# Optimization experiments

Measured on AMD Instinct MI355X. Metric: run time of the kernel, lower is better.

The kernel has to match this reference:

```python
import jax, jax.numpy as jnp
import numpy as np

N, E = 50000, 800000
D_IN, D_HID, D_OUT = 128, 128, 64
BN_EPS = 1e-5
GEN_EPS = 1e-7


def _lin_init(k, fan_in, shape):
    lim = 1.0 / np.sqrt(fan_in)
    return jax.random.uniform(k, shape, minval=-lim, maxval=lim, dtype=jnp.float32)


def setup_inputs() -> dict:
    key = jax.random.key(0)
    ks = jax.random.split(key, 12)
    x = jax.random.normal(ks[0], (N, D_IN), dtype=jnp.float32)
    edge_index = jax.random.randint(ks[1], (2, E), 0, N, dtype=jnp.int64)
    return {
        "x": x,
        # GCNConv 0 and 1 (Glorot-ish uniform init like PyG Linear)
        "W0": _lin_init(ks[2], D_IN, (D_IN, D_HID)), "b0": jnp.zeros((D_HID,), jnp.float32),
        "g0": jnp.ones((D_HID,), jnp.float32), "beta0": jnp.zeros((D_HID,), jnp.float32),
        "W1": _lin_init(ks[3], D_HID, (D_HID, D_HID)), "b1": jnp.zeros((D_HID,), jnp.float32),
        "g1": jnp.ones((D_HID,), jnp.float32), "beta1": jnp.zeros((D_HID,), jnp.float32),
        # GENConv MLP: [D_HID] -> [2*D_HID] (BN+ReLU) -> [D_OUT]
        "Wg1": _lin_init(ks[4], D_HID, (D_HID, 2 * D_HID)), "bg1": jnp.zeros((2 * D_HID,), jnp.float32),
        "gg": jnp.ones((2 * D_HID,), jnp.float32), "betag": jnp.zeros((2 * D_HID,), jnp.float32),
        "Wg2": _lin_init(ks[5], 2 * D_HID, (2 * D_HID, D_OUT)), "bg2": jnp.zeros((D_OUT,), jnp.float32),
        "edge_index": edge_index,
    }


def _bn(h, gamma, beta):
    # BatchNorm1d, training-mode batch statistics (biased variance)
    mu = jnp.mean(h, axis=0)
    var = jnp.mean(jnp.square(h - mu), axis=0)
    return (h - mu) * jax.lax.rsqrt(var + BN_EPS) * gamma + beta


def _gcn_conv(x, W, b, src, dst, n):
    # GCNConv: D^-1/2 (A + I) D^-1/2 (x W) + b
    loop = jnp.arange(n, dtype=src.dtype)
    s = jnp.concatenate([src, loop])
    d = jnp.concatenate([dst, loop])
    deg = jax.ops.segment_sum(jnp.ones_like(s, dtype=x.dtype), d, num_segments=n)
    dinv = jax.lax.rsqrt(deg)  # deg >= 1 due to self-loops
    norm = dinv[s] * dinv[d]   # [E+N]
    h = x @ W                  # [N, D]
    agg = jax.ops.segment_sum(norm[:, None] * h[s], d, num_segments=n)
    return agg + b


def _gen_conv(x, W1, b1, g, beta, W2, b2, src, dst, n):
    # GENConv (defaults): msg = relu(x_j) + eps; per-channel softmax aggregation
    # (t=1); residual add of x_dst; then MLP [D, 2D (BN+ReLU), D_out].
    msg = jax.nn.relu(x[src]) + GEN_EPS            # [E, D]
    m = jax.ops.segment_max(msg, dst, num_segments=n)
    m = jnp.where(jnp.isfinite(m), m, 0.0)         # guard zero in-degree nodes
    ex = jnp.exp(msg - m[dst])                     # [E, D]
    denom = jax.ops.segment_sum(ex, dst, num_segments=n)
    num = jax.ops.segment_sum(ex * msg, dst, num_segments=n)
    agg = num / jnp.maximum(denom, 1e-16)          # [N, D]
    out = agg + x                                  # residual
    h = jax.nn.relu(_bn(out @ W1 + b1, g, beta))
    return h @ W2 + b2


def reference(x, W0, b0, g0, beta0, W1, b1, g1, beta1,
              Wg1, bg1, gg, betag, Wg2, bg2, edge_index):
    src, dst = edge_index[0], edge_index[1]
    n = x.shape[0]
    # layer 0: GCNConv -> BN -> ReLU (dropout is identity in eval)
    h = _gcn_conv(x, W0, b0, src, dst, n)
    h = jax.nn.relu(_bn(h, g0, beta0))
    # layer 1
    h = _gcn_conv(h, W1, b1, src, dst, n)
    h = jax.nn.relu(_bn(h, g1, beta1))
    # final GENConv + log-softmax over classes
    h = _gen_conv(h, Wg1, bg1, gg, betag, Wg2, bg2, src, dst, n)
    return jax.nn.log_softmax(h, axis=-1)
```

## Files before the change

### kernel.cpp

```cpp
#include <hip/hip_runtime.h>
#include <hip/hip_bf16.h>

#define DIN 128
#define DHID 128
#define DCLS 64
#define BN_EPS 1e-5f
#define GEN_EPS 1e-7f

typedef __attribute__((ext_vector_type(8))) short short8;
typedef __attribute__((ext_vector_type(4))) float f32x4;

static __device__ __forceinline__ float bf2f(unsigned short u) {
    union { float f; unsigned int i; } x; x.i = ((unsigned int)u) << 16; return x.f;
}
static __device__ __forceinline__ unsigned short f2bf(float f) {
    union { float f; unsigned int i; } x; x.f = f;
    unsigned int r = x.i + 0x7fffu + ((x.i >> 16) & 1u);
    return (unsigned short)(r >> 16);
}
static __device__ __forceinline__ float bflo(unsigned int u) {
    union { float f; unsigned int i; } x; x.i = u << 16; return x.f;
}
static __device__ __forceinline__ float bfhi(unsigned int u) {
    union { float f; unsigned int i; } x; x.i = u & 0xffff0000u; return x.f;
}
static __device__ __forceinline__ unsigned int packbf(float lo, float hi) {
    return ((unsigned int)f2bf(hi) << 16) | f2bf(lo);
}

__global__ void k_hist(const int* __restrict__ dst, int* __restrict__ counts, int E) {
    int e = blockIdx.x * 256 + threadIdx.x;
    if (e < E) atomicAdd(&counts[dst[e]], 1);
}

__global__ __launch_bounds__(256) void k_scan1(const int* __restrict__ counts,
        int* __restrict__ roff, int* __restrict__ bsum, int N) {
    __shared__ int ls[256];
    int t = threadIdx.x;
    int base = blockIdx.x * 1024 + t * 4;
    int c0 = 0, c1 = 0, c2 = 0, c3 = 0;
    if (base + 3 < N) {
        int4 v = *(const int4*)(counts + base);
        c0 = v.x; c1 = v.y; c2 = v.z; c3 = v.w;
    } else {
        if (base + 0 < N) c0 = counts[base + 0];
        if (base + 1 < N) c1 = counts[base + 1];
        if (base + 2 < N) c2 = counts[base + 2];
        if (base + 3 < N) c3 = counts[base + 3];
    }
    ls[t] = c0 + c1 + c2 + c3;
    __syncthreads();
    for (int off = 1; off < 256; off <<= 1) {
        int v = (t >= off) ? ls[t - off] : 0;
        __syncthreads();
        ls[t] += v;
        __syncthreads();
    }
    int r = (t == 0) ? 0 : ls[t - 1];
    if (base + 0 < N) { roff[base + 0] = r; r += c0; }
    if (base + 1 < N) { roff[base + 1] = r; r += c1; }
    if (base + 2 < N) { roff[base + 2] = r; r += c2; }
    if (base + 3 < N) { roff[base + 3] = r; }
    if (t == 255) bsum[blockIdx.x] = ls[255];
}

__global__ __launch_bounds__(1024) void k_scan2(int* __restrict__ bsum, int nblk) {
    __shared__ int ls[1024];
    int t = threadIdx.x;
    ls[t] = (t < nblk) ? bsum[t] : 0;
    __syncthreads();
    for (int off = 1; off < 1024; off <<= 1) {
        int v = (t >= off) ? ls[t - off] : 0;
        __syncthreads();
        ls[t] += v;
        __syncthreads();
    }
    if (t < nblk) bsum[t] = (t == 0) ? 0 : ls[t - 1];
}

__global__ void k_scan3(const int* __restrict__ counts, const int* __restrict__ bsum,
        int* __restrict__ roff, int* __restrict__ cursor, float* __restrict__ dinv,
        int N, int E) {
    int i = blockIdx.x * 256 + threadIdx.x;
    if (i < N) {
        int r = roff[i] + bsum[i >> 10];
        roff[i] = r; cursor[i] = r;
        dinv[i] = rsqrtf((float)(counts[i] + 1));
    }
    if (i == 0) roff[N] = E;
}

__global__ void k_fill(const int* __restrict__ src, const int* __restrict__ dst,
        int* __restrict__ cursor, int* __restrict__ srcs, int E) {
    int e = blockIdx.x * 256 + threadIdx.x;
    if (e < E) {
        int d = dst[e];
        int p = atomicAdd(&cursor[d], 1);
        srcs[p] = src[e];
    }
}

__global__ void k_wt(const float* __restrict__ W, unsigned short* __restrict__ Wt, int K, int Dout) {
    int i = blockIdx.x * 256 + threadIdx.x;
    if (i >= K * Dout) return;
    int n = i / K, k = i - n * K;
    Wt[i] = f2bf(W[(size_t)k * Dout + n]);
}

template<int K, int CTILE, bool ABF16, bool OBF16, bool STATS, bool HEAD>
__global__ __launch_bounds__(256) void k_gemm(const void* __restrict__ Av,
        const unsigned short* __restrict__ Wt, const float* __restrict__ bias,
        const float* __restrict__ scale, const float* __restrict__ shift,
        const float* __restrict__ rowscale,
        void* __restrict__ Cv, float* __restrict__ gsum, float* __restrict__ gsq,
        int nrows, int Dout) {
    constexpr int KP = 136;
    constexpr int NF = CTILE / 32;
    __shared__ unsigned short smem[(64 + CTILE) * KP];
    unsigned short* sA = smem;
    unsigned short* sW = smem + 64 * KP;
    const int tid = threadIdx.x;
    const int row0 = blockIdx.x * 64, col0 = blockIdx.y * CTILE;

    const int w = tid >> 6, lane = tid & 63;
    const int wr = (w >> 1) * 32, wc = (w & 1) * (CTILE / 2);
    const int lr = lane & 15, kg = (lane >> 4) * 8;
    f32x4 acc[2][NF] = {};

    for (int kh = 0; kh < K; kh += 128) {
#pragma unroll
        for (int it = 0; it < 8; ++it) {
            int idx = (it * 256 + tid) * 4;
            int r = idx >> 7, c = idx & 127;
            int gr = row0 + r;
            float v0 = 0.f, v1 = 0.f, v2 = 0.f, v3 = 0.f;
            if (gr < nrows) {
                if (ABF16) {
                    ushort4 u = *(const ushort4*)((const unsigned short*)Av + (size_t)gr * K + kh + c);
                    v0 = bf2f(u.x); v1 = bf2f(u.y); v2 = bf2f(u.z); v3 = bf2f(u.w);
                } else {
                    float4 f = *(const float4*)((const float*)Av + (size_t)gr * K + kh + c);
                    v0 = f.x; v1 = f.y; v2 = f.z; v3 = f.w;
                }
                if (scale) {
                    int cc = kh + c;
                    v0 = fmaxf(v0 * scale[cc + 0] + shift[cc + 0], 0.f);
                    v1 = fmaxf(v1 * scale[cc + 1] + shift[cc + 1], 0.f);
                    v2 = fmaxf(v2 * scale[cc + 2] + shift[cc + 2], 0.f);
                    v3 = fmaxf(v3 * scale[cc + 3] + shift[cc + 3], 0.f);
                }
            }
            ushort4 o; o.x = f2bf(v0); o.y = f2bf(v1); o.z = f2bf(v2); o.w = f2bf(v3);
            *(ushort4*)(&sA[r * KP + c]) = o;
        }
#pragma unroll
        for (int it = 0; it < (CTILE * 128) / (256 * 8); ++it) {
            int idx = (it * 256 + tid) * 8;
            int r = idx >> 7, c = idx & 127;
            uint4 u = *(const uint4*)(Wt + (size_t)(col0 + r) * K + kh + c);
            *(uint4*)(&sW[r * KP + c]) = u;
        }
        __syncthreads();
#pragma unroll
        for (int kk = 0; kk < 128; kk += 32) {
            short8 af[2], bfr[NF];
#pragma unroll
            for (int mi = 0; mi < 2; mi++)
                af[mi] = *(const short8*)(&sA[(wr + mi * 16 + lr) * KP + kk + kg]);
#pragma unroll
            for (int ni = 0; ni < NF; ni++)
                bfr[ni] = *(const short8*)(&sW[(wc + ni * 16 + lr) * KP + kk + kg]);
#pragma unroll
            for (int mi = 0; mi < 2; mi++)
#pragma unroll
                for (int ni = 0; ni < NF; ni++)
                    acc[mi][ni] = __builtin_amdgcn_mfma_f32_16x16x32_bf16(af[mi], bfr[ni], acc[mi][ni], 0, 0, 0);
        }
        __syncthreads();
    }

    float* fs = (float*)smem;
    if (STATS) {
        if (tid < 2 * CTILE) fs[tid] = 0.f;
        __syncthreads();
    }

    float stat_s[NF], stat_q[NF];
#pragma unroll
    for (int ni = 0; ni < NF; ni++) { stat_s[ni] = 0.f; stat_q[ni] = 0.f; }

#pragma unroll
    for (int mi = 0; mi < 2; mi++) {
#pragma unroll
        for (int ni = 0; ni < NF; ni++) {
            int r = wr + mi * 16 + (lane >> 4) * 4;
            int cloc = wc + ni * 16 + (lane & 15);
            int cgl = col0 + cloc;
            float bv = bias ? bias[cgl] : 0.f;
#pragma unroll
            for (int j = 0; j < 4; j++) {
                int gr = row0 + r + j;
                if (gr < nrows) {
                    float val = acc[mi][ni][j] + bv;
                    if (rowscale) val *= rowscale[gr];
                    if (STATS) { stat_s[ni] += val; stat_q[ni] += val * val; }
                    if (HEAD) {
                        fs[(r + j) * 65 + cloc] = val;
                    } else if (OBF16) {
                        ((unsigned short*)Cv)[(size_t)gr * Dout + cgl] = f2bf(val);
                    } else {
                        ((float*)Cv)[(size_t)gr * Dout + cgl] = val;
                    }
                } else if (HEAD) {
                    fs[(r + j) * 65 + cloc] = 0.f;
                }
            }
        }
    }

    if (STATS) {
#pragma unroll
        for (int ni = 0; ni < NF; ni++) {
            int cloc = wc + ni * 16 + (lane & 15);
            atomicAdd(&fs[cloc], stat_s[ni]);
            atomicAdd(&fs[CTILE + cloc], stat_q[ni]);
        }
        __syncthreads();
        if (tid < CTILE) {
            atomicAdd(&gsum[col0 + tid], fs[tid]);
            atomicAdd(&gsq[col0 + tid], fs[CTILE + tid]);
        }
    }

    if (HEAD) {
        __syncthreads();
        for (int rr = 0; rr < 16; rr++) {
            int row = w * 16 + rr;
            int gr = row0 + row;
            if (gr >= nrows) break;
            float v = fs[row * 65 + lane];
            float m = v;
            for (int o = 32; o; o >>= 1) m = fmaxf(m, __shfl_xor(m, o));
            float e = __expf(v - m);
            float s = e;
            for (int o = 32; o; o >>= 1) s += __shfl_xor(s, o);
            ((float*)Cv)[(size_t)gr * 64 + lane] = v - m - __logf(s);
        }
    }
}

#define ACC8(u) { a0 += bflo(u.x); a1 += bfhi(u.x); a2 += bflo(u.y); a3 += bfhi(u.y); \
                  a4 += bflo(u.z); a5 += bfhi(u.z); a6 += bflo(u.w); a7 += bfhi(u.w); }

__global__ __launch_bounds__(256) void k_gcn_agg(const unsigned short* __restrict__ p,
        const int* __restrict__ roff, const int* __restrict__ srcs,
        const float* __restrict__ dinv, const float* __restrict__ b,
        unsigned short* __restrict__ out,
        float* __restrict__ gsum, float* __restrict__ gsq, int N) {
    int nw = (gridDim.x * 256) >> 6;
    int wid = (blockIdx.x * 256 + threadIdx.x) >> 6;
    int lane = threadIdx.x & 63;
    int q = lane >> 4, l16 = lane & 15;
    int c = l16 * 8;
    float4 bl = *(const float4*)(b + c);
    float4 bh = *(const float4*)(b + c + 4);
    float bb[8] = {bl.x, bl.y, bl.z, bl.w, bh.x, bh.y, bh.z, bh.w};
    float ls[8] = {0,0,0,0,0,0,0,0};
    float lq[8] = {0,0,0,0,0,0,0,0};
    for (int d = wid; d < N; d += nw) {
        float a0=0.f,a1=0.f,a2=0.f,a3=0.f,a4=0.f,a5=0.f,a6=0.f,a7=0.f;
        int e0 = roff[d], e1 = roff[d + 1];
        for (int e = e0 + q; e < e1; e += 4) {
            int s = srcs[e];
            uint4 u = ((const uint4*)(p + (size_t)s * 128))[l16];
            ACC8(u);
        }
        if (q == 0) {
            uint4 u = ((const uint4*)(p + (size_t)d * 128))[l16];
            ACC8(u);
        }
        a0 += __shfl_xor(a0,16); a0 += __shfl_xor(a0,32);
        a1 += __shfl_xor(a1,16); a1 += __shfl_xor(a1,32);
        a2 += __shfl_xor(a2,16); a2 += __shfl_xor(a2,32);
        a3 += __shfl_xor(a3,16); a3 += __shfl_xor(a3,32);
        a4 += __shfl_xor(a4,16); a4 += __shfl_xor(a4,32);
        a5 += __shfl_xor(a5,16); a5 += __shfl_xor(a5,32);
        a6 += __shfl_xor(a6,16); a6 += __shfl_xor(a6,32);
        a7 += __shfl_xor(a7,16); a7 += __shfl_xor(a7,32);
        if (q == 0) {
            float dv = dinv[d];
            float r0 = dv*a0 + bb[0], r1 = dv*a1 + bb[1];
            float r2 = dv*a2 + bb[2], r3 = dv*a3 + bb[3];
            float r4 = dv*a4 + bb[4], r5 = dv*a5 + bb[5];
            float r6 = dv*a6 + bb[6], r7 = dv*a7 + bb[7];
            ls[0]+=r0; lq[0]+=r0*r0; ls[1]+=r1; lq[1]+=r1*r1;
            ls[2]+=r2; lq[2]+=r2*r2; ls[3]+=r3; lq[3]+=r3*r3;
            ls[4]+=r4; lq[4]+=r4*r4; ls[5]+=r5; lq[5]+=r5*r5;
            ls[6]+=r6; lq[6]+=r6*r6; ls[7]+=r7; lq[7]+=r7*r7;
            uint4 o;
            o.x = packbf(r0, r1); o.y = packbf(r2, r3);
            o.z = packbf(r4, r5); o.w = packbf(r6, r7);
            ((uint4*)(out + (size_t)d * 128))[l16] = o;
        }
    }
    __shared__ float sred[4][128];
    __shared__ float qred[4][128];
    int wv = threadIdx.x >> 6;
    if (q == 0) {
#pragma unroll
        for (int k = 0; k < 8; k++) { sred[wv][c + k] = ls[k]; qred[wv][c + k] = lq[k]; }
    }
    __syncthreads();
    int t = threadIdx.x;
    if (t < 128) {
        float s = sred[0][t] + sred[1][t] + sred[2][t] + sred[3][t];
        float qq = qred[0][t] + qred[1][t] + qred[2][t] + qred[3][t];
        atomicAdd(&gsum[t], s);
        atomicAdd(&gsq[t], qq);
    }
}

__global__ __launch_bounds__(256) void k_genpre(const unsigned short* __restrict__ t4,
        const float* __restrict__ scale, const float* __restrict__ shift,
        unsigned short* __restrict__ wt, int N) {
    int i = blockIdx.x * 256 + threadIdx.x;
    int node = i >> 4, l16 = i & 15;
    if (node >= N) return;
    int c = l16 * 8;
    float4 scl = *(const float4*)(scale + c);
    float4 sch = *(const float4*)(scale + c + 4);
    float4 shl = *(const float4*)(shift + c);
    float4 shh = *(const float4*)(shift + c + 4);
    float sc[8] = {scl.x, scl.y, scl.z, scl.w, sch.x, sch.y, sch.z, sch.w};
    float sh[8] = {shl.x, shl.y, shl.z, shl.w, shh.x, shh.y, shh.z, shh.w};
    uint4 u = ((const uint4*)(t4 + (size_t)node * 128))[l16];
    float v[8] = {bflo(u.x), bfhi(u.x), bflo(u.y), bfhi(u.y),
                  bflo(u.z), bfhi(u.z), bflo(u.w), bfhi(u.w)};
    float w[8], wm[8];
#pragma unroll
    for (int k = 0; k < 8; k++) {
        float m = fmaxf(v[k] * sc[k] + sh[k], 0.f) + GEN_EPS;
        m = fminf(m, 80.f);
        w[k] = __expf(m);
        wm[k] = w[k] * m;
    }
    uint4* row = (uint4*)(wt + (size_t)node * 256);
    uint4 ow, om;
    ow.x = packbf(w[0], w[1]); ow.y = packbf(w[2], w[3]);
    ow.z = packbf(w[4], w[5]); ow.w = packbf(w[6], w[7]);
    om.x = packbf(wm[0], wm[1]); om.y = packbf(wm[2], wm[3]);
    om.z = packbf(wm[4], wm[5]); om.w = packbf(wm[6], wm[7]);
    row[l16] = ow;
    row[16 + l16] = om;
}

__global__ __launch_bounds__(256) void k_gen_agg(const unsigned short* __restrict__ t4,
        const unsigned short* __restrict__ wt,
        const int* __restrict__ roff, const int* __restrict__ srcs,
        const float* __restrict__ scale, const float* __restrict__ shift,
        unsigned short* __restrict__ out, int N) {
    int nw = (gridDim.x * 256) >> 6;
    int wid = (blockIdx.x * 256 + threadIdx.x) >> 6;
    int lane = threadIdx.x & 63;
    int q = lane >> 4, l16 = lane & 15;
    int c = l16 * 8;
    for (int d = wid; d < N; d += nw) {
        float de[8] = {0,0,0,0,0,0,0,0};
        float nu[8] = {0,0,0,0,0,0,0,0};
        int e0 = roff[d], e1 = roff[d + 1];
        for (int e = e0 + q; e < e1; e += 4) {
            int s = srcs[e];
            const uint4* row = (const uint4*)(wt + (size_t)s * 256);
            uint4 uw = row[l16];
            uint4 um = row[16 + l16];
            de[0] += bflo(uw.x); de[1] += bfhi(uw.x);
            de[2] += bflo(uw.y); de[3] += bfhi(uw.y);
            de[4] += bflo(uw.z); de[5] += bfhi(uw.z);
            de[6] += bflo(uw.w); de[7] += bfhi(uw.w);
            nu[0] += bflo(um.x); nu[1] += bfhi(um.x);
            nu[2] += bflo(um.y); nu[3] += bfhi(um.y);
            nu[4] += bflo(um.z); nu[5] += bfhi(um.z);
            nu[6] += bflo(um.w); nu[7] += bfhi(um.w);
        }
#pragma unroll
        for (int k = 0; k < 8; k++) {
            de[k] += __shfl_xor(de[k],16); de[k] += __shfl_xor(de[k],32);
            nu[k] += __shfl_xor(nu[k],16); nu[k] += __shfl_xor(nu[k],32);
        }
        if (q == 0) {
            float4 scl = *(const float4*)(scale + c);
            float4 sch = *(const float4*)(scale + c + 4);
            float4 shl = *(const float4*)(shift + c);
            float4 shh = *(const float4*)(shift + c + 4);
            float sc[8] = {scl.x, scl.y, scl.z, scl.w, sch.x, sch.y, sch.z, sch.w};
            float sh[8] = {shl.x, shl.y, shl.z, shl.w, shh.x, shh.y, shh.z, shh.w};
            uint4 u = ((const uint4*)(t4 + (size_t)d * 128))[l16];
            float v[8] = {bflo(u.x), bfhi(u.x), bflo(u.y), bfhi(u.y),
                          bflo(u.z), bfhi(u.z), bflo(u.w), bfhi(u.w)};
            float r[8];
            bool has = (e1 > e0);
#pragma unroll
            for (int k = 0; k < 8; k++) {
                float h2 = fmaxf(v[k] * sc[k] + sh[k], 0.f);
                float a = has ? nu[k] / de[k] : 0.f;
                r[k] = a + h2;
            }
            uint4 o;
            o.x = packbf(r[0], r[1]); o.y = packbf(r[2], r[3]);
            o.z = packbf(r[4], r[5]); o.w = packbf(r[6], r[7]);
            ((uint4*)(out + (size_t)d * 128))[l16] = o;
        }
    }
}

__global__ void k_fin(const float* __restrict__ sum, const float* __restrict__ sq,
        const float* __restrict__ g, const float* __restrict__ beta,
        float* __restrict__ scale, float* __restrict__ shift, int D, float invN) {
    int c = threadIdx.x;
    if (c < D) {
        float mu = sum[c] * invN;
        float var = sq[c] * invN - mu * mu;
        float s = g[c] * rsqrtf(var + BN_EPS);
        scale[c] = s;
        shift[c] = beta[c] - mu * s;
    }
}

extern "C" void kernel_launch(void* const* d_in, const int* in_sizes, int n_in,
                              void* d_out, int out_size, void* d_ws, size_t ws_size,
                              hipStream_t stream) {
    const float* x   = (const float*)d_in[0];
    const float* W0  = (const float*)d_in[1];
    const float* b0  = (const float*)d_in[2];
    const float* g0  = (const float*)d_in[3];
    const float* be0 = (const float*)d_in[4];
    const float* W1  = (const float*)d_in[5];
    const float* b1  = (const float*)d_in[6];
    const float* g1  = (const float*)d_in[7];
    const float* be1 = (const float*)d_in[8];
    const float* Wg1 = (const float*)d_in[9];
    const float* bg1 = (const float*)d_in[10];
    const float* gg  = (const float*)d_in[11];
    const float* beg = (const float*)d_in[12];
    const float* Wg2 = (const float*)d_in[13];
    const float* bg2 = (const float*)d_in[14];
    const int*   ei  = (const int*)d_in[15];

    const int N = in_sizes[0] / DIN;
    const int E = in_sizes[15] / 2;
    const int* src = ei;
    const int* dst = ei + E;

    char* ws = (char*)d_ws;
    size_t off = 0;
    auto alloc = [&](size_t b) { size_t o = off; off = (off + b + 255) & ~(size_t)255; return o; };
    size_t o_counts = alloc((size_t)N * 4);
    size_t o_stats  = alloc(1024 * 4);
    size_t o_cursor = alloc((size_t)N * 4);
    size_t o_roff   = alloc(((size_t)N + 1) * 4);
    size_t o_srcs   = alloc((size_t)E * 4);
    size_t o_dinv   = alloc((size_t)N * 4);
    size_t o_bsum   = alloc(1024 * 4);
    size_t o_ss     = alloc(1024 * 4);
    size_t o_w0t    = alloc(128 * 128 * 2);
    size_t o_w1t    = alloc(128 * 128 * 2);
    size_t o_wg1t   = alloc(256 * 128 * 2);
    size_t o_wg2t   = alloc(64 * 256 * 2);
    size_t o_xa     = alloc((size_t)N * 128 * 2);
    size_t o_xb     = alloc((size_t)N * 128 * 2);
    size_t o_c      = alloc((size_t)N * 256 * 2);
    (void)ws_size; (void)n_in; (void)out_size;

    int* counts = (int*)(ws + o_counts);
    float* stats = (float*)(ws + o_stats);
    int* cursor = (int*)(ws + o_cursor);
    int* roff = (int*)(ws + o_roff);
    int* srcs = (int*)(ws + o_srcs);
    float* dinv = (float*)(ws + o_dinv);
    int* bsum = (int*)(ws + o_bsum);
    float* ssz = (float*)(ws + o_ss);
    unsigned short* w0t  = (unsigned short*)(ws + o_w0t);
    unsigned short* w1t  = (unsigned short*)(ws + o_w1t);
    unsigned short* wg1t = (unsigned short*)(ws + o_wg1t);
    unsigned short* wg2t = (unsigned short*)(ws + o_wg2t);
    unsigned short* xa = (unsigned short*)(ws + o_xa);
    unsigned short* xb = (unsigned short*)(ws + o_xb);
    unsigned short* cb = (unsigned short*)(ws + o_c);
    unsigned short* wtab = cb;

    float* sum0 = stats;       float* sq0 = stats + 128;
    float* sum1 = stats + 256; float* sq1 = stats + 384;
    float* sumg = stats + 512; float* sqg = stats + 768;
    float* scale0 = ssz;       float* shift0 = ssz + 128;
    float* scale1 = ssz + 256; float* shift1 = ssz + 384;
    float* scaleg = ssz + 512; float* shiftg = ssz + 768;

    hipMemsetAsync(ws + o_counts, 0, o_cursor - o_counts, stream);

    int egrid = (E + 255) / 256;
    int nblk = (N + 1023) / 1024;
    k_hist<<<egrid, 256, 0, stream>>>(dst, counts, E);
    k_scan1<<<nblk, 256, 0, stream>>>(counts, roff, bsum, N);
    k_scan2<<<1, 1024, 0, stream>>>(bsum, nblk);
    k_scan3<<<(N + 255) / 256, 256, 0, stream>>>(counts, bsum, roff, cursor, dinv, N, E);
    k_fill<<<egrid, 256, 0, stream>>>(src, dst, cursor, srcs, E);

    k_wt<<<(128 * 128 + 255) / 256, 256, 0, stream>>>(W0, w0t, 128, 128);
    k_wt<<<(128 * 128 + 255) / 256, 256, 0, stream>>>(W1, w1t, 128, 128);
    k_wt<<<(128 * 256 + 255) / 256, 256, 0, stream>>>(Wg1, wg1t, 128, 256);
    k_wt<<<(256 * 64 + 255) / 256, 256, 0, stream>>>(Wg2, wg2t, 256, 64);

    int rb = (N + 63) / 64;
    const float invN = 1.f / (float)N;

    k_gemm<128, 128, false, true, false, false><<<dim3(rb, 1), 256, 0, stream>>>(
        x, w0t, nullptr, nullptr, nullptr, dinv, xa, nullptr, nullptr, N, 128);
    k_gcn_agg<<<2048, 256, 0, stream>>>(xa, roff, srcs, dinv, b0, xb, sum0, sq0, N);
    k_fin<<<1, 256, 0, stream>>>(sum0, sq0, g0, be0, scale0, shift0, 128, invN);

    k_gemm<128, 128, true, true, false, false><<<dim3(rb, 1), 256, 0, stream>>>(
        xb, w1t, nullptr, scale0, shift0, dinv, xa, nullptr, nullptr, N, 128);
    k_gcn_agg<<<2048, 256, 0, stream>>>(xa, roff, srcs, dinv, b1, xb, sum1, sq1, N);
    k_fin<<<1, 256, 0, stream>>>(sum1, sq1, g1, be1, scale1, shift1, 128, invN);

    k_genpre<<<(N * 16 + 255) / 256, 256, 0, stream>>>(xb, scale1, shift1, wtab, N);
    k_gen_agg<<<2048, 256, 0, stream>>>(xb, wtab, roff, srcs, scale1, shift1, xa, N);

    k_gemm<128, 128, true, true, true, false><<<dim3(rb, 2), 256, 0, stream>>>(
        xa, wg1t, bg1, nullptr, nullptr, nullptr, cb, sumg, sqg, N, 256);
    k_fin<<<1, 256, 0, stream>>>(sumg, sqg, gg, beg, scaleg, shiftg, 256, invN);

    k_gemm<256, 64, true, false, false, true><<<dim3(rb, 1), 256, 0, stream>>>(
        cb, wg2t, bg2, scaleg, shiftg, nullptr, d_out, nullptr, nullptr, N, 64);
}
```

Baseline: 477.7 us.

## Fold BN finalize into consumers, merge weight transposes, drop scan2, shrink GEN table

Removes the separate k_fin and k_scan2 launches: each consumer kernel now computes BN scale/shift from the raw sums into shared memory, and k_scan3 sums the block totals serially per block. The four weight-transpose launches become one kernel. The GEN softmax table now stores only exp(m) and recovers m via log in the aggregation, halving gathered bytes per edge at the cost of a log per element. Launch count and gather traffic fall, while redundant per-block BN math and extra log rounding error from bf16-stored weights are added.

Result: slower. 489.3 us (+2.4%).

```diff
diff --git a/kernel.cpp b/kernel.cpp
--- a/kernel.cpp
+++ b/kernel.cpp
@@ -64,26 +64,20 @@
     if (t == 255) bsum[blockIdx.x] = ls[255];
 }
 
-__global__ __launch_bounds__(1024) void k_scan2(int* __restrict__ bsum, int nblk) {
-    __shared__ int ls[1024];
-    int t = threadIdx.x;
-    ls[t] = (t < nblk) ? bsum[t] : 0;
-    __syncthreads();
-    for (int off = 1; off < 1024; off <<= 1) {
-        int v = (t >= off) ? ls[t - off] : 0;
-        __syncthreads();
-        ls[t] += v;
-        __syncthreads();
-    }
-    if (t < nblk) bsum[t] = (t == 0) ? 0 : ls[t - 1];
-}
-
 __global__ void k_scan3(const int* __restrict__ counts, const int* __restrict__ bsum,
         int* __restrict__ roff, int* __restrict__ cursor, float* __restrict__ dinv,
         int N, int E) {
+    __shared__ int sbase;
+    if (threadIdx.x == 0) {
+        int blk = (blockIdx.x * 256) >> 10;
+        int s = 0;
+        for (int j = 0; j < blk; j++) s += bsum[j];
+        sbase = s;
+    }
+    __syncthreads();
     int i = blockIdx.x * 256 + threadIdx.x;
     if (i < N) {
-        int r = roff[i] + bsum[i >> 10];
+        int r = roff[i] + sbase;
         roff[i] = r; cursor[i] = r;
         dinv[i] = rsqrtf((float)(counts[i] + 1));
     }
@@ -100,27 +94,48 @@
     }
 }
 
-__global__ void k_wt(const float* __restrict__ W, unsigned short* __restrict__ Wt, int K, int Dout) {
+__global__ void k_wt_all(const float* __restrict__ W0, const float* __restrict__ W1,
+        const float* __restrict__ Wg1, const float* __restrict__ Wg2,
+        unsigned short* __restrict__ w0t, unsigned short* __restrict__ w1t,
+        unsigned short* __restrict__ wg1t, unsigned short* __restrict__ wg2t) {
     int i = blockIdx.x * 256 + threadIdx.x;
-    if (i >= K * Dout) return;
-    int n = i / K, k = i - n * K;
-    Wt[i] = f2bf(W[(size_t)k * Dout + n]);
-}
-
-template<int K, int CTILE, bool ABF16, bool OBF16, bool STATS, bool HEAD>
+    const float* W; unsigned short* Wt; int Kk, Dd, j;
+    if (i < 16384)      { W = W0;  Wt = w0t;  Kk = 128; Dd = 128; j = i; }
+    else if (i < 32768) { W = W1;  Wt = w1t;  Kk = 128; Dd = 128; j = i - 16384; }
+    else if (i < 65536) { W = Wg1; Wt = wg1t; Kk = 128; Dd = 256; j = i - 32768; }
+    else if (i < 81920) { W = Wg2; Wt = wg2t; Kk = 256; Dd = 64;  j = i - 65536; }
+    else return;
+    int n = j / Kk, k = j - n * Kk;
+    Wt[j] = f2bf(W[(size_t)k * Dd + n]);
+}
+
+template<int K, int CTILE, bool ABF16, bool OBF16, bool STATS, bool HEAD, bool SFIN>
 __global__ __launch_bounds__(256) void k_gemm(const void* __restrict__ Av,
         const unsigned short* __restrict__ Wt, const float* __restrict__ bias,
-        const float* __restrict__ scale, const float* __restrict__ shift,
+        const float* __restrict__ bnsum, const float* __restrict__ bnsq,
+        const float* __restrict__ bng, const float* __restrict__ bnbeta, float invN,
         const float* __restrict__ rowscale,
         void* __restrict__ Cv, float* __restrict__ gsum, float* __restrict__ gsq,
         int nrows, int Dout) {
     constexpr int KP = 136;
     constexpr int NF = CTILE / 32;
+    constexpr int BNSZ = SFIN ? 2 * K : 2;
     __shared__ unsigned short smem[(64 + CTILE) * KP];
+    __shared__ float sBN[BNSZ];
     unsigned short* sA = smem;
     unsigned short* sW = smem + 64 * KP;
     const int tid = threadIdx.x;
     const int row0 = blockIdx.x * 64, col0 = blockIdx.y * CTILE;
+
+    if (SFIN) {
+        for (int c = tid; c < K; c += 256) {
+            float mu = bnsum[c] * invN;
+            float var = bnsq[c] * invN - mu * mu;
+            float s = bng[c] * rsqrtf(var + BN_EPS);
+            sBN[c] = s; sBN[K + c] = bnbeta[c] - mu * s;
+        }
+        __syncthreads();
+    }
 
     const int w = tid >> 6, lane = tid & 63;
     const int wr = (w >> 1) * 32, wc = (w & 1) * (CTILE / 2);
@@ -142,12 +157,12 @@
                     float4 f = *(const float4*)((const float*)Av + (size_t)gr * K + kh + c);
                     v0 = f.x; v1 = f.y; v2 = f.z; v3 = f.w;
                 }
-                if (scale) {
+                if (SFIN) {
                     int cc = kh + c;
-                    v0 = fmaxf(v0 * scale[cc + 0] + shift[cc + 0], 0.f);
-                    v1 = fmaxf(v1 * scale[cc + 1] + shift[cc + 1], 0.f);
-                    v2 = fmaxf(v2 * scale[cc + 2] + shift[cc + 2], 0.f);
-                    v3 = fmaxf(v3 * scale[cc + 3] + shift[cc + 3], 0.f);
+                    v0 = fmaxf(v0 * sBN[cc + 0] + sBN[K + cc + 0], 0.f);
+                    v1 = fmaxf(v1 * sBN[cc + 1] + sBN[K + cc + 1], 0.f);
+                    v2 = fmaxf(v2 * sBN[cc + 2] + sBN[K + cc + 2], 0.f);
+                    v3 = fmaxf(v3 * sBN[cc + 3] + sBN[K + cc + 3], 0.f);
                 }
             }
             ushort4 o; o.x = f2bf(v0); o.y = f2bf(v1); o.z = f2bf(v2); o.w = f2bf(v3);
@@ -321,47 +336,56 @@
 }
 
 __global__ __launch_bounds__(256) void k_genpre(const unsigned short* __restrict__ t4,
-        const float* __restrict__ scale, const float* __restrict__ shift,
+        const float* __restrict__ bnsum, const float* __restrict__ bnsq,
+        const float* __restrict__ bng, const float* __restrict__ bnbeta, float invN,
         unsigned short* __restrict__ wt, int N) {
-    int i = blockIdx.x * 256 + threadIdx.x;
+    __shared__ float ssc[128], ssh[128];
+    int tid = threadIdx.x;
+    if (tid < 128) {
+        float mu = bnsum[tid] * invN;
+        float var = bnsq[tid] * invN - mu * mu;
+        float s = bng[tid] * rsqrtf(var + BN_EPS);
+        ssc[tid] = s; ssh[tid] = bnbeta[tid] - mu * s;
+    }
+    __syncthreads();
+    int i = blockIdx.x * 256 + tid;
     int node = i >> 4, l16 = i & 15;
     if (node >= N) return;
     int c = l16 * 8;
-    float4 scl = *(const float4*)(scale + c);
-    float4 sch = *(const float4*)(scale + c + 4);
-    float4 shl = *(const float4*)(shift + c);
-    float4 shh = *(const float4*)(shift + c + 4);
-    float sc[8] = {scl.x, scl.y, scl.z, scl.w, sch.x, sch.y, sch.z, sch.w};
-    float sh[8] = {shl.x, shl.y, shl.z, shl.w, shh.x, shh.y, shh.z, shh.w};
     uint4 u = ((const uint4*)(t4 + (size_t)node * 128))[l16];
     float v[8] = {bflo(u.x), bfhi(u.x), bflo(u.y), bfhi(u.y),
                   bflo(u.z), bfhi(u.z), bflo(u.w), bfhi(u.w)};
-    float w[8], wm[8];
+    float w[8];
 #pragma unroll
     for (int k = 0; k < 8; k++) {
-        float m = fmaxf(v[k] * sc[k] + sh[k], 0.f) + GEN_EPS;
+        float m = fmaxf(v[k] * ssc[c + k] + ssh[c + k], 0.f) + GEN_EPS;
         m = fminf(m, 80.f);
         w[k] = __expf(m);
-        wm[k] = w[k] * m;
-    }
-    uint4* row = (uint4*)(wt + (size_t)node * 256);
-    uint4 ow, om;
+    }
+    uint4 ow;
     ow.x = packbf(w[0], w[1]); ow.y = packbf(w[2], w[3]);
     ow.z = packbf(w[4], w[5]); ow.w = packbf(w[6], w[7]);
-    om.x = packbf(wm[0], wm[1]); om.y = packbf(wm[2], wm[3]);
-    om.z = packbf(wm[4], wm[5]); om.w = packbf(wm[6], wm[7]);
-    row[l16] = ow;
-    row[16 + l16] = om;
+    ((uint4*)(wt + (size_t)node * 128))[l16] = ow;
 }
 
 __global__ __launch_bounds__(256) void k_gen_agg(const unsigned short* __restrict__ t4,
         const unsigned short* __restrict__ wt,
         const int* __restrict__ roff, const int* __restrict__ srcs,
-        const float* __restrict__ scale, const float* __restrict__ shift,
+        const float* __restrict__ bnsum, const float* __restrict__ bnsq,
+        const float* __restrict__ bng, const float* __restrict__ bnbeta, float invN,
         unsigned short* __restrict__ out, int N) {
+    __shared__ float ssc[128], ssh[128];
+    int tid = threadIdx.x;
+    if (tid < 128) {
+        float mu = bnsum[tid] * invN;
+        float var = bnsq[tid] * invN - mu * mu;
+        float s = bng[tid] * rsqrtf(var + BN_EPS);
+        ssc[tid] = s; ssh[tid] = bnbeta[tid] - mu * s;
+    }
+    __syncthreads();
     int nw = (gridDim.x * 256) >> 6;
-    int wid = (blockIdx.x * 256 + threadIdx.x) >> 6;
-    int lane = threadIdx.x & 63;
+    int wid = (blockIdx.x * 256 + tid) >> 6;
+    int lane = tid & 63;
     int q = lane >> 4, l16 = lane & 15;
     int c = l16 * 8;
     for (int d = wid; d < N; d += nw) {
@@ -370,17 +394,17 @@
         int e0 = roff[d], e1 = roff[d + 1];
         for (int e = e0 + q; e < e1; e += 4) {
             int s = srcs[e];
-            const uint4* row = (const uint4*)(wt + (size_t)s * 256);
-            uint4 uw = row[l16];
-            uint4 um = row[16 + l16];
-            de[0] += bflo(uw.x); de[1] += bfhi(uw.x);
-            de[2] += bflo(uw.y); de[3] += bfhi(uw.y);
-            de[4] += bflo(uw.z); de[5] += bfhi(uw.z);
-            de[6] += bflo(uw.w); de[7] += bfhi(uw.w);
-            nu[0] += bflo(um.x); nu[1] += bfhi(um.x);
-            nu[2] += bflo(um.y); nu[3] += bfhi(um.y);
-            nu[4] += bflo(um.z); nu[5] += bfhi(um.z);
-            nu[6] += bflo(um.w); nu[7] += bfhi(um.w);
+            uint4 u = ((const uint4*)(wt + (size_t)s * 128))[l16];
+            float w0 = bflo(u.x), w1 = bfhi(u.x), w2 = bflo(u.y), w3 = bfhi(u.y);
+            float w4 = bflo(u.z), w5 = bfhi(u.z), w6 = bflo(u.w), w7 = bfhi(u.w);
+            de[0] += w0; nu[0] += w0 * __logf(w0);
+            de[1] += w1; nu[1] += w1 * __logf(w1);
+            de[2] += w2; nu[2] += w2 * __logf(w2);
+            de[3] += w3; nu[3] += w3 * __logf(w3);
+            de[4] += w4; nu[4] += w4 * __logf(w4);
+            de[5] += w5; nu[5] += w5 * __logf(w5);
+            de[6] += w6; nu[6] += w6 * __logf(w6);
+            de[7] += w7; nu[7] += w7 * __logf(w7);
         }
 #pragma unroll
         for (int k = 0; k < 8; k++) {
@@ -388,12 +412,6 @@
             nu[k] += __shfl_xor(nu[k],16); nu[k] += __shfl_xor(nu[k],32);
         }
         if (q == 0) {
-            float4 scl = *(const float4*)(scale + c);
-            float4 sch = *(const float4*)(scale + c + 4);
-            float4 shl = *(const float4*)(shift + c);
-            float4 shh = *(const float4*)(shift + c + 4);
-            float sc[8] = {scl.x, scl.y, scl.z, scl.w, sch.x, sch.y, sch.z, sch.w};
-            float sh[8] = {shl.x, shl.y, shl.z, shl.w, shh.x, shh.y, shh.z, shh.w};
             uint4 u = ((const uint4*)(t4 + (size_t)d * 128))[l16];
             float v[8] = {bflo(u.x), bfhi(u.x), bflo(u.y), bfhi(u.y),
                           bflo(u.z), bfhi(u.z), bflo(u.w), bfhi(u.w)};
@@ -401,7 +419,7 @@
             bool has = (e1 > e0);
 #pragma unroll
             for (int k = 0; k < 8; k++) {
-                float h2 = fmaxf(v[k] * sc[k] + sh[k], 0.f);
+                float h2 = fmaxf(v[k] * ssc[c + k] + ssh[c + k], 0.f);
                 float a = has ? nu[k] / de[k] : 0.f;
                 r[k] = a + h2;
             }
@@ -410,19 +428,6 @@
             o.z = packbf(r[4], r[5]); o.w = packbf(r[6], r[7]);
             ((uint4*)(out + (size_t)d * 128))[l16] = o;
         }
-    }
-}
-
-__global__ void k_fin(const float* __restrict__ sum, const float* __restrict__ sq,
-        const float* __restrict__ g, const float* __restrict__ beta,
-        float* __restrict__ scale, float* __restrict__ shift, int D, float invN) {
-    int c = threadIdx.x;
-    if (c < D) {
-        float mu = sum[c] * invN;
-        float var = sq[c] * invN - mu * mu;
-        float s = g[c] * rsqrtf(var + BN_EPS);
-        scale[c] = s;
-        shift[c] = beta[c] - mu * s;
     }
 }
 
@@ -461,7 +466,6 @@
     size_t o_srcs   = alloc((size_t)E * 4);
     size_t o_dinv   = alloc((size_t)N * 4);
     size_t o_bsum   = alloc(1024 * 4);
-    size_t o_ss     = alloc(1024 * 4);
     size_t o_w0t    = alloc(128 * 128 * 2);
     size_t o_w1t    = alloc(128 * 128 * 2);
     size_t o_wg1t   = alloc(256 * 128 * 2);
@@ -478,7 +482,6 @@
     int* srcs = (int*)(ws + o_srcs);
     float* dinv = (float*)(ws + o_dinv);
     int* bsum = (int*)(ws + o_bsum);
-    float* ssz = (float*)(ws + o_ss);
     unsigned short* w0t  = (unsigned short*)(ws + o_w0t);
     unsigned short* w1t  = (unsigned short*)(ws + o_w1t);
     unsigned short* wg1t = (unsigned short*)(ws + o_wg1t);
@@ -491,9 +494,6 @@
     float* sum0 = stats;       float* sq0 = stats + 128;
     float* sum1 = stats + 256; float* sq1 = stats + 384;
     float* sumg = stats + 512; float* sqg = stats + 768;
-    float* scale0 = ssz;       float* shift0 = ssz + 128;
-    float* scale1 = ssz + 256; float* shift1 = ssz + 384;
-    float* scaleg = ssz + 512; float* shiftg = ssz + 768;
 
     hipMemsetAsync(ws + o_counts, 0, o_cursor - o_counts, stream);
 
@@ -501,35 +501,28 @@
     int nblk = (N + 1023) / 1024;
     k_hist<<<egrid, 256, 0, stream>>>(dst, counts, E);
     k_scan1<<<nblk, 256, 0, stream>>>(counts, roff, bsum, N);
-    k_scan2<<<1, 1024, 0, stream>>>(bsum, nblk);
     k_scan3<<<(N + 255) / 256, 256, 0, stream>>>(counts, bsum, roff, cursor, dinv, N, E);
     k_fill<<<egrid, 256, 0, stream>>>(src, dst, cursor, srcs, E);
 
-    k_wt<<<(128 * 128 + 255) / 256, 256, 0, stream>>>(W0, w0t, 128, 128);
-    k_wt<<<(128 * 128 + 255) / 256, 256, 0, stream>>>(W1, w1t, 128, 128);
-    k_wt<<<(128 * 256 + 255) / 256, 256, 0, stream>>>(Wg1, wg1t, 128, 256);
-    k_wt<<<(256 * 64 + 255) / 256, 256, 0, stream>>>(Wg2, wg2t, 256, 64);
+    k_wt_all<<<320, 256, 0, stream>>>(W0, W1, Wg1, Wg2, w0t, w1t, wg1t, wg2t);
 
     int rb = (N + 63) / 64;
     const float invN = 1.f / (float)N;
 
-    k_gemm<128, 128, false, true, false, false><<<dim3(rb, 1), 256, 0, stream>>>(
-        x, w0t, nullptr, nullptr, nullptr, dinv, xa, nullptr, nullptr, N, 128);
+    k_gemm<128, 128, false, true, false, false, false><<<dim3(rb, 1), 256, 0, stream>>>(
+        x, w0t, nullptr, nullptr, nullptr, nullptr, nullptr, 0.f, dinv, xa, nullptr, nullptr, N, 128);
     k_gcn_agg<<<2048, 256, 0, stream>>>(xa, roff, srcs, dinv, b0, xb, sum0, sq0, N);
-    k_fin<<<1, 256, 0, stream>>>(sum0, sq0, g0, be0, scale0, shift0, 128, invN);
-
-    k_gemm<128, 128, true, true, false, false><<<dim3(rb, 1), 256, 0, stream>>>(
-        xb, w1t, nullptr, scale0, shift0, dinv, xa, nullptr, nullptr, N, 128);
+
+    k_gemm<128, 128, true, true, false, false, true><<<dim3(rb, 1), 256, 0, stream>>>(
+        xb, w1t, nullptr, sum0, sq0, g0, be0, invN, dinv, xa, nullptr, nullptr, N, 128);
     k_gcn_agg<<<2048, 256, 0, stream>>>(xa, roff, srcs, dinv, b1, xb, sum1, sq1, N);
-    k_fin<<<1, 256, 0, stream>>>(sum1, sq1, g1, be1, scale1, shift1, 128, invN);
-
-    k_genpre<<<(N * 16 + 255) / 256, 256, 0, stream>>>(xb, scale1, shift1, wtab, N);
-    k_gen_agg<<<2048, 256, 0, stream>>>(xb, wtab, roff, srcs, scale1, shift1, xa, N);
-
-    k_gemm<128, 128, true, true, true, false><<<dim3(rb, 2), 256, 0, stream>>>(
-        xa, wg1t, bg1, nullptr, nullptr, nullptr, cb, sumg, sqg, N, 256);
-    k_fin<<<1, 256, 0, stream>>>(sumg, sqg, gg, beg, scaleg, shiftg, 256, invN);
-
-    k_gemm<256, 64, true, false, false, true><<<dim3(rb, 1), 256, 0, stream>>>(
-        cb, wg2t, bg2, scaleg, shiftg, nullptr, d_out, nullptr, nullptr, N, 64);
-}
+
+    k_genpre<<<(N * 16 + 255) / 256, 256, 0, stream>>>(xb, sum1, sq1, g1, be1, invN, wtab, N);
+    k_gen_agg<<<2048, 256, 0, stream>>>(xb, wtab, roff, srcs, sum1, sq1, g1, be1, invN, xa, N);
+
+    k_gemm<128, 128, true, true, true, false, false><<<dim3(rb, 2), 256, 0, stream>>>(
+        xa, wg1t, bg1, nullptr, nullptr, nullptr, nullptr, 0.f, nullptr, cb, sumg, sqg, N, 256);
+
+    k_gemm<256, 64, true, false, false, true, true><<<dim3(rb, 1), 256, 0, stream>>>(
+        cb, wg2t, bg2, sumg, sqg, gg, beg, invN, nullptr, d_out, nullptr, nullptr, N, 64);
+}
```
